# Optimization experiments

Measured on AMD Instinct MI355X. Metric: run time of the kernel, lower is better.

## Reference

```python
import jax, jax.numpy as jnp
import numpy as np

NEG_INF = -1e9
LRELU_SLOPE = 0.2  # torch GAT default leaky_relu negative slope


def setup_inputs() -> dict:
    key = jax.random.key(0)
    k1, k2, k3, k4, k5 = jax.random.split(key, 5)
    N, F_IN, H, DH = 4096, 1433, 8, 8  # n_nodes, in_features, n_heads, per-head dim (n_hidden=64)
    vert = jax.random.normal(k1, (N, F_IN), dtype=jnp.float32)
    edge = jax.random.randint(k2, (N, N), 0, 2, dtype=jnp.int32)  # dense adjacency mask
    W = jax.random.normal(k3, (F_IN, H * DH), dtype=jnp.float32) * 0.05
    a_l = jax.random.normal(k4, (H, DH), dtype=jnp.float32) * 0.05
    a_r = jax.random.normal(k5, (H, DH), dtype=jnp.float32) * 0.05
    return {"vert": vert, "edge": edge, "W": W, "a_l": a_l, "a_r": a_r}


def reference(vert, edge, W, a_l, a_r):
    # GAT-style edge-affinity layer (is_concat=True) + ELU; dropout is identity (eval mode).
    N = vert.shape[0]
    H, DH = a_l.shape
    g = (vert @ W).reshape(N, H, DH)                      # [N,H,Dh] projected node features
    sl = jnp.einsum('nhd,hd->nh', g, a_l)                 # source-node attention term
    sr = jnp.einsum('nhd,hd->nh', g, a_r)                 # target-node attention term
    e = sl[:, None, :] + sr[None, :, :]                   # [N,N,H]: attn([g_i || g_j])
    e = jnp.where(e >= 0, e, LRELU_SLOPE * e)             # leaky_relu
    mask = (edge != 0)[:, :, None]                        # [N,N,1]
    e = jnp.where(mask, e, NEG_INF)                       # mask non-edges
    a = jax.nn.softmax(e, axis=1)                         # normalize over neighbors j
    out = jnp.einsum('ijh,jhd->ihd', a, g).reshape(N, H * DH)  # aggregate + concat heads
    return jax.nn.elu(out)
```

## Files before the change

### kernel.cpp

```cpp
#include <hip/hip_runtime.h>
#include <hip/hip_bf16.h>

#define NN 4096
#define FIN 1433
#define NH 8
#define DH 8
#define HD 64
#define KP 1472
#define LOG2E 1.44269504f
#define NJS 8
#define NCHK ((NN / NJS) / 64)
#define NKS 4

typedef unsigned int u32;
typedef unsigned long long u64;
typedef float v4f __attribute__((ext_vector_type(4)));
typedef _Float16 f16;
typedef _Float16 h2 __attribute__((ext_vector_type(2)));
typedef _Float16 f16x8 __attribute__((ext_vector_type(8)));

static __device__ __forceinline__ short f2h16(float f) {
    union { f16 h; short s; } u; u.h = (f16)f; return u.s;
}
static __device__ __forceinline__ h2 u2h2(u32 x) {
    union { u32 u; h2 h; } v; v.u = x; return v.h;
}
static __device__ __forceinline__ u32 h22u(h2 x) {
    union { h2 h; u32 u; } v; v.h = x; return v.u;
}

#if __has_builtin(__builtin_amdgcn_sbfe)
#define SBFE1(x, k) __builtin_amdgcn_sbfe((int)(x), (k), 1)
#else
#define SBFE1(x, k) (((int)((x) << (31 - (k)))) >> 31)
#endif

static __device__ __forceinline__ void gload_lds16(const void* g, void* l) {
    __builtin_amdgcn_global_load_lds(
        (const __attribute__((address_space(1))) void*)g,
        (__attribute__((address_space(3))) void*)l, 16, 0, 0);
}

__global__ __launch_bounds__(256) void k_wprep(const float* __restrict__ W,
                                               short* __restrict__ Wt) {
    __shared__ float Ts[64][65];
    const int c = blockIdx.x;
    const int u = threadIdx.x;
    const int n4 = (u & 15) * 4;
    const int kr = u >> 4;
#pragma unroll
    for (int q = 0; q < 4; ++q) {
        const int kl = kr + q * 16;
        const int kg = c * 64 + kl;
        v4f v = {0.f, 0.f, 0.f, 0.f};
        if (kg < FIN) v = *(const v4f*)&W[(size_t)kg * HD + n4];
        *(v4f*)&Ts[kl][n4] = v;
    }
    __syncthreads();
    const int n = u >> 2;
    const int koff = (u & 3) * 16;
    __align__(16) short tmp[16];
#pragma unroll
    for (int r = 0; r < 16; ++r) tmp[r] = f2h16(Ts[koff + r][n]);
    *(uint4*)&Wt[(size_t)n * KP + c * 64 + koff]     = *(uint4*)&tmp[0];
    *(uint4*)&Wt[(size_t)n * KP + c * 64 + koff + 8] = *(uint4*)&tmp[8];
}

__global__ __launch_bounds__(256, 4) void k_mid(
    const float* __restrict__ vert, const short* __restrict__ Wt,
    const int* __restrict__ edge,
    float* __restrict__ Cp, uint4* __restrict__ emask)
{
    __shared__ float cacc[4][16][68];

    const int t = threadIdx.x, lane = t & 63, w = t >> 6;
    const int ml = lane & 15, q = lane >> 4;
    const int ib = blockIdx.x;
    const int ks = blockIdx.y;
    const int i0 = ib * 16;

    {
        const int b = ks * 256 + ib;
        for (int r = 0; r < 4; ++r) {
            const int row = b * 4 + r;
            const int* erow = edge + (size_t)row * NN;
            uint4* mrow = emask + (size_t)row * (NN / 128);
#pragma unroll
            for (int it = 0; it < 8; ++it) {
                const int ck = w * 8 + it;
                const int2 e2 = *(const int2*)&erow[ck * 128 + 2 * lane];
                const u64 bA = __ballot(e2.x != 0);
                const u64 bB = __ballot(e2.y != 0);
                if (lane == 0)
                    mrow[ck] = (uint4){(u32)bA, (u32)bB,
                                       (u32)(bA >> 32), (u32)(bB >> 32)};
            }
        }
    }

    const float* vrow = vert + (size_t)(i0 + ml) * FIN;
    v4f acc[4];
#pragma unroll
    for (int g = 0; g < 4; ++g) acc[g] = (v4f){0.f, 0.f, 0.f, 0.f};

    for (int c = ks + 4 * w; c < 45; c += 16) {
        const int k0 = c * 32 + q * 8;
        v4f a0, a1;
        if (k0 + 7 < FIN) {
            a0 = *(const v4f*)&vrow[k0];
            a1 = *(const v4f*)&vrow[k0 + 4];
        } else {
            float tmp[8];
#pragma unroll
            for (int e = 0; e < 8; ++e)
                tmp[e] = (k0 + e < FIN) ? vrow[k0 + e] : 0.f;
            a0 = (v4f){tmp[0], tmp[1], tmp[2], tmp[3]};
            a1 = (v4f){tmp[4], tmp[5], tmp[6], tmp[7]};
        }
        const f16x8 af = {(f16)a0.x, (f16)a0.y, (f16)a0.z, (f16)a0.w,
                          (f16)a1.x, (f16)a1.y, (f16)a1.z, (f16)a1.w};
#pragma unroll
        for (int g = 0; g < 4; ++g) {
            const f16x8 bf = *(const f16x8*)&Wt[(size_t)(g * 16 + ml) * KP + k0];
            acc[g] = __builtin_amdgcn_mfma_f32_16x16x32_f16(af, bf, acc[g], 0, 0, 0);
        }
    }

#pragma unroll
    for (int g = 0; g < 4; ++g)
#pragma unroll
        for (int r = 0; r < 4; ++r)
            cacc[w][q * 4 + r][g * 16 + ml] = acc[g][r];
    __syncthreads();

    const int m = t >> 4, n4 = (t & 15) * 4;
    v4f s = (v4f){0.f, 0.f, 0.f, 0.f};
#pragma unroll
    for (int ww = 0; ww < 4; ++ww) s += *(const v4f*)&cacc[ww][m][n4];
    *(v4f*)&Cp[((size_t)ks * NN + i0 + m) * HD + n4] = s;
}

__global__ __launch_bounds__(256) void k_gpost(
    const float* __restrict__ Cp,
    const float* __restrict__ al, const float* __restrict__ ar,
    short* __restrict__ gT, short* __restrict__ eB, short* __restrict__ eD,
    float* __restrict__ Rw)
{
    const int t = threadIdx.x;
    const int gid = blockIdx.x * 256 + t;
    const int i = gid >> 4, n4 = (gid & 15) * 4;

    v4f s = (v4f){0.f, 0.f, 0.f, 0.f};
#pragma unroll
    for (int ks = 0; ks < NKS; ++ks)
        s += *(const v4f*)&Cp[((size_t)ks * NN + i) * HD + n4];

#pragma unroll
    for (int e = 0; e < 4; ++e)
        gT[(size_t)(n4 + e) * NN + i] = f2h16(s[e]);

    float pl = s.x * al[n4] + s.y * al[n4 + 1] + s.z * al[n4 + 2] + s.w * al[n4 + 3];
    float pr = s.x * ar[n4] + s.y * ar[n4 + 1] + s.z * ar[n4 + 2] + s.w * ar[n4 + 3];
    pl += __shfl_xor(pl, 1, 64);
    pr += __shfl_xor(pr, 1, 64);
    if ((t & 1) == 0) {
        const int h = (t & 15) >> 1;
        eB[h * NN + i] = f2h16(exp2f(pr * LOG2E));
        eD[h * NN + i] = f2h16(exp2f(0.2f * pr * LOG2E));
        Rw[i * NH + h] = exp2f(-0.8f * pl * LOG2E);
    }
}

__global__ __launch_bounds__(256, 8) void k_attn(
    const uint4* __restrict__ emask, const short* __restrict__ gT,
    const short* __restrict__ eB, const short* __restrict__ eD,
    const float* __restrict__ Rw,
    float* __restrict__ numw, float* __restrict__ denw)
{
    __shared__ __align__(16) short Gs[2][64 * 64];
    __shared__ __align__(16) short BDs[2][8 * 128];

    const int t = threadIdx.x, lane = t & 63, w = t >> 6;
    const int ml = lane & 15, quad = lane >> 4;
    const int m8 = ml & 7;
    const int i0 = blockIdx.x * 16;
    const int js = blockIdx.y;
    const int jbase = js * (NN / NJS);
    const int h0 = w, h1 = w + 4;
    const int qb4 = quad * 4;
    const bool mhi = (ml >= 8);
    const u32 one2 = 0x3C003C00u;
    const uint4 ones4 = (uint4){one2, one2, one2, one2};

    h2 Ri[2];
    {
        const f16 r0 = (f16)Rw[(i0 + ml) * NH + h0];
        const f16 r1 = (f16)Rw[(i0 + ml) * NH + h1];
        Ri[0] = (h2){r0, r0};
        Ri[1] = (h2){r1, r1};
    }

    const uint2* mrow = (const uint2*)emask + (size_t)(i0 + ml) * (NN / 64) + js * NCHK;

    const short *gsrc0, *gsrc1;
    {
        int u = t, row = u >> 3;
        gsrc0 = gT + (size_t)row * NN + jbase + (((u & 7) * 8) ^ ((row & 7) * 8));
        u = 256 + t; row = u >> 3;
        gsrc1 = gT + (size_t)row * NN + jbase + (((u & 7) * 8) ^ ((row & 7) * 8));
    }
    const short* bdsrc = nullptr;
    if (t < 128) {
        const int head = t >> 4, slot = t & 15;
        bdsrc = (slot < 8 ? eB : eD) + (size_t)head * NN + jbase + (slot & 7) * 8;
    }
    const int wub = (t & ~63) * 16;

#define STAGE(buf, ck)                                                        \
    do {                                                                      \
        const int jc_ = (ck) * 64;                                            \
        gload_lds16(gsrc0 + jc_, (char*)Gs[buf] + wub);                       \
        gload_lds16(gsrc1 + jc_, (char*)Gs[buf] + 4096 + wub);                \
        if (t < 128) gload_lds16(bdsrc + jc_, (char*)BDs[buf] + wub);         \
    } while (0)

    v4f acc[2];
    acc[0] = (v4f){0.f, 0.f, 0.f, 0.f};
    acc[1] = (v4f){0.f, 0.f, 0.f, 0.f};

    STAGE(0, 0);
    uint2 mw = mrow[0], pm;

    for (int c = 0; c < NCHK; ++c) {
        const int cb = c & 1, nb = cb ^ 1;
        __syncthreads();
        const bool pf = (c + 1) < NCHK;
        if (pf) { STAGE(nb, c + 1); pm = mrow[c + 1]; }
#pragma unroll
        for (int s = 0; s < 2; ++s) {
            const int xj = s * 32 + quad * 8;
            const int xg = xj ^ (m8 * 8);
            const uint4 gu0 = *(const uint4*)&Gs[cb][(h0 * 8 + m8) * 64 + xg];
            const uint4 gu1 = *(const uint4*)&Gs[cb][(h1 * 8 + m8) * 64 + xg];
            const uint4 bu0 = *(const uint4*)&BDs[cb][h0 * 128 + xj];
            const uint4 du0 = *(const uint4*)&BDs[cb][h0 * 128 + 64 + xj];
            const uint4 bu1 = *(const uint4*)&BDs[cb][h1 * 128 + xj];
            const uint4 du1 = *(const uint4*)&BDs[cb][h1 * 128 + 64 + xj];
            const int base = (s << 4) + qb4;
            const u32 WA = mw.x >> base;
            const u32 WB = mw.y >> base;
            u32 m[4];
#pragma unroll
            for (int k = 0; k < 4; ++k) {
                const int ea = SBFE1(WA, k);
                const int eb = SBFE1(WB, k);
                m[k] = __builtin_amdgcn_perm((u32)eb, (u32)ea, 0x05040100u);
            }
            u32 aw0[4], aw1[4];
#pragma unroll
            for (int k = 0; k < 4; ++k) {
                const u32 rd0 = h22u(Ri[0] * u2h2((&du0.x)[k]));
                const u32 rd1 = h22u(Ri[1] * u2h2((&du1.x)[k]));
                u32 p0, p1;
                asm("v_pk_max_f16 %0, %1, %2" : "=v"(p0) : "v"(rd0), "v"((&bu0.x)[k]));
                asm("v_pk_max_f16 %0, %1, %2" : "=v"(p1) : "v"(rd1), "v"((&bu1.x)[k]));
                aw0[k] = p0 & m[k];
                aw1[k] = p1 & m[k];
            }
            union { uint4 u; f16x8 h; } a0u, a1u, g0u, g1u;
            a0u.u = (uint4){aw0[0], aw0[1], aw0[2], aw0[3]};
            a1u.u = (uint4){aw1[0], aw1[1], aw1[2], aw1[3]};
            g0u.u = mhi ? ones4 : gu0;
            g1u.u = mhi ? ones4 : gu1;
            acc[0] = __builtin_amdgcn_mfma_f32_16x16x32_f16(a0u.h, g0u.h, acc[0], 0, 0, 0);
            acc[1] = __builtin_amdgcn_mfma_f32_16x16x32_f16(a1u.h, g1u.h, acc[1], 0, 0, 0);
        }
        if (pf) mw = pm;
    }
#undef STAGE

    float* nw = numw + (size_t)js * NN * HD;
    float* dw = denw + (size_t)js * NN * NH;
    const int ibase = i0 + quad * 4;
#pragma unroll
    for (int hh = 0; hh < 2; ++hh) {
        const int h = w + hh * 4;
#pragma unroll
        for (int r = 0; r < 4; ++r) {
            if (ml < 8)       nw[(ibase + r) * HD + h * 8 + ml] = acc[hh][r];
            else if (ml == 8) dw[(ibase + r) * NH + h]          = acc[hh][r];
        }
    }
}

__global__ __launch_bounds__(256) void k_comb(
    const float* __restrict__ numw, const float* __restrict__ denw,
    float* __restrict__ out)
{
    const int gid = blockIdx.x * 256 + threadIdx.x;
    const int i = gid >> 6, h = (gid & 63) >> 3;
    float num = 0.f, den = 0.f;
#pragma unroll
    for (int s = 0; s < NJS; ++s) {
        num += numw[(size_t)s * NN * HD + gid];
        den += denw[(size_t)s * NN * NH + i * NH + h];
    }
    float x = num / den;
    out[gid] = (x > 0.f) ? x : (__expf(x) - 1.f);
}

extern "C" void kernel_launch(void* const* d_in, const int* in_sizes, int n_in,
                              void* d_out, int out_size, void* d_ws, size_t ws_size,
                              hipStream_t stream) {
    const float* vert = (const float*)d_in[0];
    const int*   edge = (const int*)d_in[1];
    const float* W    = (const float*)d_in[2];
    const float* al   = (const float*)d_in[3];
    const float* ar   = (const float*)d_in[4];
    float* out = (float*)d_out;

    char* ws = (char*)d_ws;
    short* gT    = (short*)ws;
    short* eB    = (short*)(ws + 512 * 1024);
    short* eD    = (short*)(ws + 576 * 1024);
    float* Rw    = (float*)(ws + 640 * 1024);
    short* Wt    = (short*)(ws + 768 * 1024);
    uint4* emask = (uint4*)(ws + 1024 * 1024);
    float* Cp    = (float*)(ws + 3 * 1024 * 1024);
    float* numw  = (float*)(ws + 7 * 1024 * 1024);
    float* denw  = (float*)(ws + 15 * 1024 * 1024);

    hipLaunchKernelGGL(k_wprep, dim3(23), dim3(256), 0, stream, W, Wt);
    hipLaunchKernelGGL(k_mid, dim3(NN / 16, NKS), dim3(256), 0, stream,
                       vert, Wt, edge, Cp, emask);
    hipLaunchKernelGGL(k_gpost, dim3(NN * 16 / 256), dim3(256), 0, stream,
                       Cp, al, ar, gT, eB, eD, Rw);
    hipLaunchKernelGGL(k_attn, dim3(NN / 16, NJS), dim3(256), 0, stream,
                       emask, gT, eB, eD, Rw, numw, denw);
    hipLaunchKernelGGL(k_comb, dim3(NN * HD / 256), dim3(256), 0, stream,
                       numw, denw, out);
}
```

Baseline: 167.0 us.

## Split edge-mask packing into own kernel and double i-rows per attention block

Moves the edge adjacency bit-packing out of the projection GEMM kernel into a separate k_eprep kernel, so the GEMM kernel only does the matmul. The attention kernel now handles 32 target rows per block instead of 16, reusing each staged G and exp-factor tile in LDS for two MFMA sub-tiles. This halves the LDS staging traffic per row but raises register use and lowers the occupancy bound from 8 to 4 blocks. The extra kernel launch also removes the overlap the edge pass previously had with the GEMM.

```diff
diff --git a/kernel.cpp b/kernel.cpp
--- a/kernel.cpp
+++ b/kernel.cpp
@@ -9,6 +9,7 @@
 #define KP 1472
 #define LOG2E 1.44269504f
 #define NJS 8
+#define ITB 32
 #define NCHK ((NN / NJS) / 64)
 #define NKS 4
 
@@ -39,6 +40,23 @@
     __builtin_amdgcn_global_load_lds(
         (const __attribute__((address_space(1))) void*)g,
         (__attribute__((address_space(3))) void*)l, 16, 0, 0);
+}
+
+__global__ __launch_bounds__(256) void k_eprep(const int* __restrict__ edge,
+                                               uint4* __restrict__ emask) {
+    const int t = threadIdx.x, lane = t & 63, w = t >> 6;
+    const int row = blockIdx.x;
+    const int* erow = edge + (size_t)row * NN;
+    uint4* mrow = emask + (size_t)row * (NN / 128);
+#pragma unroll
+    for (int it = 0; it < 8; ++it) {
+        const int ck = w * 8 + it;
+        const int2 e2 = *(const int2*)&erow[ck * 128 + 2 * lane];
+        const u64 bA = __ballot(e2.x != 0);
+        const u64 bB = __ballot(e2.y != 0);
+        if (lane == 0)
+            mrow[ck] = (uint4){(u32)bA, (u32)bB, (u32)(bA >> 32), (u32)(bB >> 32)};
+    }
 }
 
 __global__ __launch_bounds__(256) void k_wprep(const float* __restrict__ W,
@@ -66,39 +84,18 @@
     *(uint4*)&Wt[(size_t)n * KP + c * 64 + koff + 8] = *(uint4*)&tmp[8];
 }
 
-__global__ __launch_bounds__(256, 4) void k_mid(
+__global__ __launch_bounds__(256, 4) void k_gemm(
     const float* __restrict__ vert, const short* __restrict__ Wt,
-    const int* __restrict__ edge,
-    float* __restrict__ Cp, uint4* __restrict__ emask)
+    float* __restrict__ Cp)
 {
     __shared__ float cacc[4][16][68];
 
     const int t = threadIdx.x, lane = t & 63, w = t >> 6;
     const int ml = lane & 15, q = lane >> 4;
-    const int ib = blockIdx.x;
+    const int i0 = blockIdx.x * 16;
     const int ks = blockIdx.y;
-    const int i0 = ib * 16;
-
-    {
-        const int b = ks * 256 + ib;
-        for (int r = 0; r < 4; ++r) {
-            const int row = b * 4 + r;
-            const int* erow = edge + (size_t)row * NN;
-            uint4* mrow = emask + (size_t)row * (NN / 128);
-#pragma unroll
-            for (int it = 0; it < 8; ++it) {
-                const int ck = w * 8 + it;
-                const int2 e2 = *(const int2*)&erow[ck * 128 + 2 * lane];
-                const u64 bA = __ballot(e2.x != 0);
-                const u64 bB = __ballot(e2.y != 0);
-                if (lane == 0)
-                    mrow[ck] = (uint4){(u32)bA, (u32)bB,
-                                       (u32)(bA >> 32), (u32)(bB >> 32)};
-            }
-        }
-    }
-
     const float* vrow = vert + (size_t)(i0 + ml) * FIN;
+
     v4f acc[4];
 #pragma unroll
     for (int g = 0; g < 4; ++g) acc[g] = (v4f){0.f, 0.f, 0.f, 0.f};
@@ -171,7 +168,7 @@
     }
 }
 
-__global__ __launch_bounds__(256, 8) void k_attn(
+__global__ __launch_bounds__(256, 4) void k_attn(
     const uint4* __restrict__ emask, const short* __restrict__ gT,
     const short* __restrict__ eB, const short* __restrict__ eD,
     const float* __restrict__ Rw,
@@ -183,7 +180,7 @@
     const int t = threadIdx.x, lane = t & 63, w = t >> 6;
     const int ml = lane & 15, quad = lane >> 4;
     const int m8 = ml & 7;
-    const int i0 = blockIdx.x * 16;
+    const int i0 = blockIdx.x * ITB;
     const int js = blockIdx.y;
     const int jbase = js * (NN / NJS);
     const int h0 = w, h1 = w + 4;
@@ -192,15 +189,17 @@
     const u32 one2 = 0x3C003C00u;
     const uint4 ones4 = (uint4){one2, one2, one2, one2};
 
-    h2 Ri[2];
-    {
-        const f16 r0 = (f16)Rw[(i0 + ml) * NH + h0];
-        const f16 r1 = (f16)Rw[(i0 + ml) * NH + h1];
-        Ri[0] = (h2){r0, r0};
-        Ri[1] = (h2){r1, r1};
-    }
-
-    const uint2* mrow = (const uint2*)emask + (size_t)(i0 + ml) * (NN / 64) + js * NCHK;
+    h2 Ri[2][2];
+#pragma unroll
+    for (int sub = 0; sub < 2; ++sub) {
+        const f16 r0 = (f16)Rw[(i0 + sub * 16 + ml) * NH + h0];
+        const f16 r1 = (f16)Rw[(i0 + sub * 16 + ml) * NH + h1];
+        Ri[sub][0] = (h2){r0, r0};
+        Ri[sub][1] = (h2){r1, r1};
+    }
+
+    const uint2* mrow0 = (const uint2*)emask + (size_t)(i0 + ml) * (NN / 64) + js * NCHK;
+    const uint2* mrow1 = (const uint2*)emask + (size_t)(i0 + 16 + ml) * (NN / 64) + js * NCHK;
 
     const short *gsrc0, *gsrc1;
     {
@@ -224,71 +223,85 @@
         if (t < 128) gload_lds16(bdsrc + jc_, (char*)BDs[buf] + wub);         \
     } while (0)
 
-    v4f acc[2];
-    acc[0] = (v4f){0.f, 0.f, 0.f, 0.f};
-    acc[1] = (v4f){0.f, 0.f, 0.f, 0.f};
+    v4f acc[2][2];
+#pragma unroll
+    for (int sub = 0; sub < 2; ++sub) {
+        acc[sub][0] = (v4f){0.f, 0.f, 0.f, 0.f};
+        acc[sub][1] = (v4f){0.f, 0.f, 0.f, 0.f};
+    }
 
     STAGE(0, 0);
-    uint2 mw = mrow[0], pm;
+    uint2 mw0 = mrow0[0], mw1 = mrow1[0], pm0, pm1;
 
     for (int c = 0; c < NCHK; ++c) {
         const int cb = c & 1, nb = cb ^ 1;
         __syncthreads();
         const bool pf = (c + 1) < NCHK;
-        if (pf) { STAGE(nb, c + 1); pm = mrow[c + 1]; }
+        if (pf) {
+            STAGE(nb, c + 1);
+            pm0 = mrow0[c + 1];
+            pm1 = mrow1[c + 1];
+        }
 #pragma unroll
         for (int s = 0; s < 2; ++s) {
             const int xj = s * 32 + quad * 8;
             const int xg = xj ^ (m8 * 8);
-            const uint4 gu0 = *(const uint4*)&Gs[cb][(h0 * 8 + m8) * 64 + xg];
-            const uint4 gu1 = *(const uint4*)&Gs[cb][(h1 * 8 + m8) * 64 + xg];
+            union { uint4 u; f16x8 h; } g0u, g1u;
+            g0u.u = mhi ? ones4 : *(const uint4*)&Gs[cb][(h0 * 8 + m8) * 64 + xg];
+            g1u.u = mhi ? ones4 : *(const uint4*)&Gs[cb][(h1 * 8 + m8) * 64 + xg];
             const uint4 bu0 = *(const uint4*)&BDs[cb][h0 * 128 + xj];
             const uint4 du0 = *(const uint4*)&BDs[cb][h0 * 128 + 64 + xj];
             const uint4 bu1 = *(const uint4*)&BDs[cb][h1 * 128 + xj];
             const uint4 du1 = *(const uint4*)&BDs[cb][h1 * 128 + 64 + xj];
             const int base = (s << 4) + qb4;
-            const u32 WA = mw.x >> base;
-            const u32 WB = mw.y >> base;
-            u32 m[4];
-#pragma unroll
-            for (int k = 0; k < 4; ++k) {
-                const int ea = SBFE1(WA, k);
-                const int eb = SBFE1(WB, k);
-                m[k] = __builtin_amdgcn_perm((u32)eb, (u32)ea, 0x05040100u);
+#pragma unroll
+            for (int sub = 0; sub < 2; ++sub) {
+                const u32 WA = (sub ? mw1.x : mw0.x) >> base;
+                const u32 WB = (sub ? mw1.y : mw0.y) >> base;
+                u32 m[4];
+#pragma unroll
+                for (int k = 0; k < 4; ++k) {
+                    const int ea = SBFE1(WA, k);
+                    const int eb = SBFE1(WB, k);
+                    m[k] = __builtin_amdgcn_perm((u32)eb, (u32)ea, 0x05040100u);
+                }
+                u32 aw0[4], aw1[4];
+#pragma unroll
+                for (int k = 0; k < 4; ++k) {
+                    const u32 rd0 = h22u(Ri[sub][0] * u2h2((&du0.x)[k]));
+                    const u32 rd1 = h22u(Ri[sub][1] * u2h2((&du1.x)[k]));
+                    u32 p0, p1;
+                    asm("v_pk_max_f16 %0, %1, %2" : "=v"(p0) : "v"(rd0), "v"((&bu0.x)[k]));
+                    asm("v_pk_max_f16 %0, %1, %2" : "=v"(p1) : "v"(rd1), "v"((&bu1.x)[k]));
+                    aw0[k] = p0 & m[k];
+                    aw1[k] = p1 & m[k];
+                }
+                union { uint4 u; f16x8 h; } a0u, a1u;
+                a0u.u = (uint4){aw0[0], aw0[1], aw0[2], aw0[3]};
+                a1u.u = (uint4){aw1[0], aw1[1], aw1[2], aw1[3]};
+                acc[sub][0] = __builtin_amdgcn_mfma_f32_16x16x32_f16(
+                    a0u.h, g0u.h, acc[sub][0], 0, 0, 0);
+                acc[sub][1] = __builtin_amdgcn_mfma_f32_16x16x32_f16(
+                    a1u.h, g1u.h, acc[sub][1], 0, 0, 0);
             }
-            u32 aw0[4], aw1[4];
-#pragma unroll
-            for (int k = 0; k < 4; ++k) {
-                const u32 rd0 = h22u(Ri[0] * u2h2((&du0.x)[k]));
-                const u32 rd1 = h22u(Ri[1] * u2h2((&du1.x)[k]));
-                u32 p0, p1;
-                asm("v_pk_max_f16 %0, %1, %2" : "=v"(p0) : "v"(rd0), "v"((&bu0.x)[k]));
-                asm("v_pk_max_f16 %0, %1, %2" : "=v"(p1) : "v"(rd1), "v"((&bu1.x)[k]));
-                aw0[k] = p0 & m[k];
-                aw1[k] = p1 & m[k];
-            }
-            union { uint4 u; f16x8 h; } a0u, a1u, g0u, g1u;
-            a0u.u = (uint4){aw0[0], aw0[1], aw0[2], aw0[3]};
-            a1u.u = (uint4){aw1[0], aw1[1], aw1[2], aw1[3]};
-            g0u.u = mhi ? ones4 : gu0;
-            g1u.u = mhi ? ones4 : gu1;
-            acc[0] = __builtin_amdgcn_mfma_f32_16x16x32_f16(a0u.h, g0u.h, acc[0], 0, 0, 0);
-            acc[1] = __builtin_amdgcn_mfma_f32_16x16x32_f16(a1u.h, g1u.h, acc[1], 0, 0, 0);
-        }
-        if (pf) mw = pm;
+        }
+        if (pf) { mw0 = pm0; mw1 = pm1; }
     }
 #undef STAGE
 
     float* nw = numw + (size_t)js * NN * HD;
     float* dw = denw + (size_t)js * NN * NH;
-    const int ibase = i0 + quad * 4;
-#pragma unroll
-    for (int hh = 0; hh < 2; ++hh) {
-        const int h = w + hh * 4;
-#pragma unroll
-        for (int r = 0; r < 4; ++r) {
-            if (ml < 8)       nw[(ibase + r) * HD + h * 8 + ml] = acc[hh][r];
-            else if (ml == 8) dw[(ibase + r) * NH + h]          = acc[hh][r];
+#pragma unroll
+    for (int sub = 0; sub < 2; ++sub) {
+        const int ibase = i0 + sub * 16 + quad * 4;
+#pragma unroll
+        for (int hh = 0; hh < 2; ++hh) {
+            const int h = w + hh * 4;
+#pragma unroll
+            for (int r = 0; r < 4; ++r) {
+                if (ml < 8)       nw[(ibase + r) * HD + h * 8 + ml] = acc[sub][hh][r];
+                else if (ml == 8) dw[(ibase + r) * NH + h]          = acc[sub][hh][r];
+            }
         }
     }
 }
@@ -330,12 +343,13 @@
     float* numw  = (float*)(ws + 7 * 1024 * 1024);
     float* denw  = (float*)(ws + 15 * 1024 * 1024);
 
+    hipLaunchKernelGGL(k_eprep, dim3(NN), dim3(256), 0, stream, edge, emask);
     hipLaunchKernelGGL(k_wprep, dim3(23), dim3(256), 0, stream, W, Wt);
-    hipLaunchKernelGGL(k_mid, dim3(NN / 16, NKS), dim3(256), 0, stream,
-                       vert, Wt, edge, Cp, emask);
+    hipLaunchKernelGGL(k_gemm, dim3(NN / 16, NKS), dim3(256), 0, stream,
+                       vert, Wt, Cp);
     hipLaunchKernelGGL(k_gpost, dim3(NN * 16 / 256), dim3(256), 0, stream,
                        Cp, al, ar, gT, eB, eD, Rw);
-    hipLaunchKernelGGL(k_attn, dim3(NN / 16, NJS), dim3(256), 0, stream,
+    hipLaunchKernelGGL(k_attn, dim3(NN / ITB, NJS), dim3(256), 0, stream,
                        emask, gT, eB, eD, Rw, numw, denw);
     hipLaunchKernelGGL(k_comb, dim3(NN * HD / 256), dim3(256), 0, stream,
                        numw, denw, out);
```

Result: faster. 154.8 us (-7.3%).
